# Kernel optimization log

Hardware: AMD Instinct MI355X
Metric: run time of the kernel (lower is better)

## Reference

```python
import jax, jax.numpy as jnp
import numpy as np

EMBED_DIM = 1024
NUM_HEADS = 16
HEAD_DIM = EMBED_DIM // NUM_HEADS


def layer_norm(x, gamma, beta, eps=1e-5):
    mu = jnp.mean(x, axis=-1, keepdims=True)
    var = jnp.var(x, axis=-1, keepdims=True)
    return (x - mu) * jax.lax.rsqrt(var + eps) * gamma + beta


def setup_inputs() -> dict:
    key = jax.random.key(0)
    ks = jax.random.split(key, 8)
    D = EMBED_DIM
    s = 1.0 / np.sqrt(D)
    x = jax.random.normal(ks[0], (2, 2048, D), dtype=jnp.float32)
    Wq = jax.random.uniform(ks[1], (D, D), jnp.float32, -s, s)
    Wk = jax.random.uniform(ks[2], (D, D), jnp.float32, -s, s)
    Wv = jax.random.uniform(ks[3], (D, D), jnp.float32, -s, s)
    W1 = jax.random.uniform(ks[4], (D, 4 * D), jnp.float32, -s, s)
    b1 = jnp.zeros((4 * D,), jnp.float32)
    W2 = jax.random.uniform(ks[5], (4 * D, D), jnp.float32, -1.0 / np.sqrt(4 * D), 1.0 / np.sqrt(4 * D))
    b2 = jnp.zeros((D,), jnp.float32)
    g1 = jnp.ones((D,), jnp.float32); be1 = jnp.zeros((D,), jnp.float32)
    g2 = jnp.ones((D,), jnp.float32); be2 = jnp.zeros((D,), jnp.float32)
    return {"x": x, "Wq": Wq, "Wk": Wk, "Wv": Wv, "W1": W1, "b1": b1,
            "W2": W2, "b2": b2, "g1": g1, "be1": be1, "g2": g2, "be2": be2}


def reference(x, Wq, Wk, Wv, W1, b1, W2, b2, g1, be1, g2, be2):
    B, S, D = x.shape
    H, Hd = NUM_HEADS, HEAD_DIM
    x_norm = layer_norm(x, g1, be1)
    # QKV projections (no bias), split into heads: [B, H, S, Hd]
    q = (x_norm @ Wq).reshape(B, S, H, Hd).transpose(0, 2, 1, 3)
    k = (x_norm @ Wk).reshape(B, S, H, Hd).transpose(0, 2, 1, 3)
    v = (x_norm @ Wv).reshape(B, S, H, Hd).transpose(0, 2, 1, 3)
    energy = jnp.einsum('bhqd,bhkd->bhqk', q, k)
    attn = jax.nn.softmax(energy / jnp.sqrt(jnp.float32(Hd)), axis=-1)
    out = jnp.einsum('bhqk,bhkd->bhqd', attn, v)
    attention = out.transpose(0, 2, 1, 3).reshape(B, S, D)
    x_res = attention + x
    x_norm2 = layer_norm(x_res, g2, be2)
    # Faithful quirk: FFN applied to x_res (not x_norm2)
    ffn_out = jax.nn.relu(x_res @ W1 + b1) @ W2 + b2
    return ffn_out + x_norm2
```

## Files before the change

kernel.cpp:

```cpp
#include <hip/hip_runtime.h>
#include <hip/hip_bf16.h>
#include <stdint.h>

typedef __hip_bfloat16 bf16;
typedef __attribute__((ext_vector_type(4))) float f32x4;
typedef __attribute__((ext_vector_type(8))) short s16x8;
typedef __attribute__((ext_vector_type(4))) short s16x4;

#define DEV static __device__ __forceinline__

DEV short f2bf(float f) {
  bf16 h = __float2bfloat16(f);
  short s;
  __builtin_memcpy(&s, &h, 2);
  return s;
}
DEV float bf2f(short s) {
  bf16 h;
  __builtin_memcpy(&h, &s, 2);
  return __bfloat162float(h);
}

__global__ __launch_bounds__(256) void transpose_cvt(
    const float* __restrict__ W, bf16* __restrict__ Wt, int K, int N)
{
  __shared__ float tile[32][33];
  const int n0 = blockIdx.x << 5;
  const int k0 = blockIdx.y << 5;
  const int tx = threadIdx.x & 31, ty = threadIdx.x >> 5;
#pragma unroll
  for (int i = 0; i < 4; ++i)
    tile[ty + i * 8][tx] = W[(size_t)(k0 + ty + i * 8) * N + n0 + tx];
  __syncthreads();
#pragma unroll
  for (int i = 0; i < 4; ++i)
    Wt[(size_t)(n0 + ty + i * 8) * K + k0 + tx] = __float2bfloat16(tile[tx][ty + i * 8]);
}

__global__ __launch_bounds__(256) void ln_bf16(
    const float* __restrict__ x, const float* __restrict__ g,
    const float* __restrict__ be, bf16* __restrict__ out)
{
  const int t = threadIdx.x;
  const size_t row = blockIdx.x;
  const float4 v = ((const float4*)(x + row * 1024))[t];
  float s = v.x + v.y + v.z + v.w;
  float ss = v.x * v.x + v.y * v.y + v.z * v.z + v.w * v.w;
#pragma unroll
  for (int off = 32; off > 0; off >>= 1) {
    s += __shfl_down(s, off);
    ss += __shfl_down(ss, off);
  }
  __shared__ float sh[8];
  const int wave = t >> 6, lane = t & 63;
  if (!lane) { sh[wave] = s; sh[4 + wave] = ss; }
  __syncthreads();
  s = sh[0] + sh[1] + sh[2] + sh[3];
  ss = sh[4] + sh[5] + sh[6] + sh[7];
  const float mean = s * (1.f / 1024.f);
  const float rstd = rsqrtf(ss * (1.f / 1024.f) - mean * mean + 1e-5f);
  const float4 gv = ((const float4*)g)[t];
  const float4 bv = ((const float4*)be)[t];
  s16x4 o;
  o[0] = f2bf((v.x - mean) * rstd * gv.x + bv.x);
  o[1] = f2bf((v.y - mean) * rstd * gv.y + bv.y);
  o[2] = f2bf((v.z - mean) * rstd * gv.z + bv.z);
  o[3] = f2bf((v.w - mean) * rstd * gv.w + bv.w);
  ((s16x4*)(out + row * 1024))[t] = o;
}

__global__ __launch_bounds__(256) void add_ln_bf16(
    const float* __restrict__ a, const float* __restrict__ x,
    const float* __restrict__ g, const float* __restrict__ be,
    bf16* __restrict__ xres, bf16* __restrict__ xnorm)
{
  const int t = threadIdx.x;
  const size_t row = blockIdx.x;
  const float4 av = ((const float4*)(a + row * 1024))[t];
  const float4 xv = ((const float4*)(x + row * 1024))[t];
  float4 v;
  v.x = av.x + xv.x; v.y = av.y + xv.y; v.z = av.z + xv.z; v.w = av.w + xv.w;
  float s = v.x + v.y + v.z + v.w;
  float ss = v.x * v.x + v.y * v.y + v.z * v.z + v.w * v.w;
#pragma unroll
  for (int off = 32; off > 0; off >>= 1) {
    s += __shfl_down(s, off);
    ss += __shfl_down(ss, off);
  }
  __shared__ float sh[8];
  const int wave = t >> 6, lane = t & 63;
  if (!lane) { sh[wave] = s; sh[4 + wave] = ss; }
  __syncthreads();
  s = sh[0] + sh[1] + sh[2] + sh[3];
  ss = sh[4] + sh[5] + sh[6] + sh[7];
  const float mean = s * (1.f / 1024.f);
  const float rstd = rsqrtf(ss * (1.f / 1024.f) - mean * mean + 1e-5f);
  const float4 gv = ((const float4*)g)[t];
  const float4 bv = ((const float4*)be)[t];
  s16x4 r, o;
  r[0] = f2bf(v.x); r[1] = f2bf(v.y); r[2] = f2bf(v.z); r[3] = f2bf(v.w);
  o[0] = f2bf((v.x - mean) * rstd * gv.x + bv.x);
  o[1] = f2bf((v.y - mean) * rstd * gv.y + bv.y);
  o[2] = f2bf((v.z - mean) * rstd * gv.z + bv.z);
  o[3] = f2bf((v.w - mean) * rstd * gv.w + bv.w);
  ((s16x4*)(xres + row * 1024))[t] = r;
  ((s16x4*)(xnorm + row * 1024))[t] = o;
}

template <int EPI>
__global__ __launch_bounds__(256) void gemm_bt(
    const bf16* __restrict__ A, const bf16* __restrict__ Bt,
    void* __restrict__ C, const float* __restrict__ bias,
    const bf16* __restrict__ add_bf16, int M, int N, int K)
{
  __shared__ bf16 sA0[128 * 64];
  __shared__ bf16 sB0[128 * 64];
  __shared__ bf16 sA1[128 * 64];
  __shared__ bf16 sB1[128 * 64];
  const int tid = threadIdx.x;
  const int wave = tid >> 6, lane = tid & 63;
  const int fr = lane & 15, fg = lane >> 4;
  const int f7 = fr & 7;
  const int wr = wave >> 1, wc = wave & 1;
  const int nbx = N >> 7;
  int bid = blockIdx.x;
  if ((gridDim.x & 7) == 0) {
    const int cpx = gridDim.x >> 3;
    bid = (bid & 7) * cpx + (bid >> 3);
  }
  const int brow = (bid / nbx) << 7;
  const int bcol = (bid % nbx) << 7;

  f32x4 acc[4][4] = {};

  const int rsub = lane >> 3;
  const int cl = (lane & 7) ^ rsub;
  size_t ga[4], gb[4];
  int la[4];
#pragma unroll
  for (int j = 0; j < 4; ++j) {
    const int r = wave * 32 + j * 8;
    ga[j] = (size_t)(brow + r + rsub) * K + cl * 8;
    gb[j] = (size_t)(bcol + r + rsub) * K + cl * 8;
    la[j] = r * 64;
  }

#define GSTAGE(SA, SB, kt)                                                     \
  do {                                                                         \
    _Pragma("unroll")                                                          \
    for (int jj = 0; jj < 4; ++jj) {                                           \
      __builtin_amdgcn_global_load_lds(                                        \
          (const __attribute__((address_space(1))) uint32_t*)(A + ga[jj] + (kt)), \
          (__attribute__((address_space(3))) uint32_t*)(&SA[la[jj]]), 16, 0, 0);  \
      __builtin_amdgcn_global_load_lds(                                        \
          (const __attribute__((address_space(1))) uint32_t*)(Bt + gb[jj] + (kt)),\
          (__attribute__((address_space(3))) uint32_t*)(&SB[la[jj]]), 16, 0, 0);  \
    }                                                                          \
  } while (0)

#define COMPUTE(SA, SB)                                                        \
  do {                                                                         \
    s16x8 af[4][2], bfr[4][2];                                                 \
    _Pragma("unroll")                                                          \
    for (int m = 0; m < 4; ++m)                                                \
      _Pragma("unroll")                                                        \
      for (int kk = 0; kk < 2; ++kk)                                           \
        af[m][kk] = *(const s16x8*)(&SA[(wr * 64 + m * 16 + fr) * 64 +         \
                                        (((kk * 4 + fg) ^ f7) << 3)]);         \
    _Pragma("unroll")                                                          \
    for (int n = 0; n < 4; ++n)                                                \
      _Pragma("unroll")                                                        \
      for (int kk = 0; kk < 2; ++kk)                                           \
        bfr[n][kk] = *(const s16x8*)(&SB[(wc * 64 + n * 16 + fr) * 64 +        \
                                         (((kk * 4 + fg) ^ f7) << 3)]);        \
    _Pragma("unroll")                                                          \
    for (int kk = 0; kk < 2; ++kk)                                             \
      _Pragma("unroll")                                                        \
      for (int m = 0; m < 4; ++m)                                              \
        _Pragma("unroll")                                                      \
        for (int n = 0; n < 4; ++n)                                            \
          acc[m][n] = __builtin_amdgcn_mfma_f32_16x16x32_bf16(                 \
              af[m][kk], bfr[n][kk], acc[m][n], 0, 0, 0);                      \
  } while (0)

  GSTAGE(sA0, sB0, 0);
  __syncthreads();

  int kt = 0;
  for (;;) {
    if (kt + 64 < K) {
      GSTAGE(sA1, sB1, kt + 64);
      COMPUTE(sA0, sB0);
      __syncthreads();
    } else {
      COMPUTE(sA0, sB0);
      break;
    }
    kt += 64;
    if (kt + 64 < K) {
      GSTAGE(sA0, sB0, kt + 64);
      COMPUTE(sA1, sB1);
      __syncthreads();
    } else {
      COMPUTE(sA1, sB1);
      break;
    }
    kt += 64;
  }
#undef GSTAGE
#undef COMPUTE

  const int crow = brow + wr * 64;
  const int ccol = bcol + wc * 64;
#pragma unroll
  for (int m = 0; m < 4; ++m) {
#pragma unroll
    for (int n = 0; n < 4; ++n) {
      const int col = ccol + n * 16 + fr;
#pragma unroll
      for (int j = 0; j < 4; ++j) {
        const int row = crow + m * 16 + fg * 4 + j;
        float v = acc[m][n][j];
        if (EPI == 0) {
          ((bf16*)C)[(size_t)row * N + col] = __float2bfloat16(v);
        } else if (EPI == 1) {
          v += bias[col];
          v = fmaxf(v, 0.f);
          ((bf16*)C)[(size_t)row * N + col] = __float2bfloat16(v);
        } else {
          float a;
          {
            bf16 hb = add_bf16[(size_t)row * N + col];
            a = __bfloat162float(hb);
          }
          ((float*)C)[(size_t)row * N + col] = v + bias[col] + a;
        }
      }
    }
  }
}

template <int EPI>
__global__ __launch_bounds__(512) void gemm512_bt(
    const bf16* __restrict__ A, const bf16* __restrict__ Bt,
    void* __restrict__ C, const float* __restrict__ bias, int M, int N, int K)
{
  __shared__ bf16 sA[3][256 * 64];
  __shared__ bf16 sB[3][128 * 64];
  const int tid = threadIdx.x;
  const int wave = tid >> 6, lane = tid & 63;
  const int fr = lane & 15, fg = lane >> 4;
  const int f7 = fr & 7;
  const int wr = wave >> 1, wc = wave & 1;
  const int nbx = N >> 7;
  int bid = blockIdx.x;
  if ((gridDim.x & 7) == 0) {
    const int cpx = gridDim.x >> 3;
    bid = (bid & 7) * cpx + (bid >> 3);
  }
  const int brow = (bid / nbx) << 8;
  const int bcol = (bid % nbx) << 7;

  f32x4 acc[4][4] = {};

  const int rsub = lane >> 3;
  const int cl = (lane & 7) ^ rsub;
  size_t ga[4], gb[2];
  int laA[4], laB[2];
#pragma unroll
  for (int j = 0; j < 4; ++j) {
    const int r = j * 64 + wave * 8;
    ga[j] = (size_t)(brow + r + rsub) * K + cl * 8;
    laA[j] = r * 64;
  }
#pragma unroll
  for (int j = 0; j < 2; ++j) {
    const int r = j * 64 + wave * 8;
    gb[j] = (size_t)(bcol + r + rsub) * K + cl * 8;
    laB[j] = r * 64;
  }

#define STG(bi, koff)                                                          \
  do {                                                                         \
    _Pragma("unroll")                                                          \
    for (int jj = 0; jj < 4; ++jj)                                             \
      __builtin_amdgcn_global_load_lds(                                        \
          (const __attribute__((address_space(1))) uint32_t*)(A + ga[jj] + (koff)), \
          (__attribute__((address_space(3))) uint32_t*)(&sA[bi][laA[jj]]), 16, 0, 0); \
    _Pragma("unroll")                                                          \
    for (int jj = 0; jj < 2; ++jj)                                             \
      __builtin_amdgcn_global_load_lds(                                        \
          (const __attribute__((address_space(1))) uint32_t*)(Bt + gb[jj] + (koff)),\
          (__attribute__((address_space(3))) uint32_t*)(&sB[bi][laB[jj]]), 16, 0, 0); \
  } while (0)

  const int nk = K >> 6;
  STG(0, 0);
  STG(1, 64);

  int cb = 0;
  for (int j = 0; j < nk; ++j) {
    if (j < nk - 1) {
      asm volatile("s_waitcnt vmcnt(6)" ::: "memory");
    } else {
      asm volatile("s_waitcnt vmcnt(0)" ::: "memory");
    }
    __builtin_amdgcn_s_barrier();
    if (j + 2 < nk) {
      const int tb = (cb + 2) % 3;
      STG(tb, (j + 2) * 64);
    }
    const bf16* SA = sA[cb];
    const bf16* SB = sB[cb];
    s16x8 af[4][2], bfr[4][2];
#pragma unroll
    for (int m = 0; m < 4; ++m)
#pragma unroll
      for (int kk = 0; kk < 2; ++kk)
        af[m][kk] = *(const s16x8*)(&SA[(wr * 64 + m * 16 + fr) * 64 +
                                        (((kk * 4 + fg) ^ f7) << 3)]);
#pragma unroll
    for (int n = 0; n < 4; ++n)
#pragma unroll
      for (int kk = 0; kk < 2; ++kk)
        bfr[n][kk] = *(const s16x8*)(&SB[(wc * 64 + n * 16 + fr) * 64 +
                                         (((kk * 4 + fg) ^ f7) << 3)]);
    __builtin_amdgcn_s_setprio(1);
#pragma unroll
    for (int kk = 0; kk < 2; ++kk)
#pragma unroll
      for (int m = 0; m < 4; ++m)
#pragma unroll
        for (int n = 0; n < 4; ++n)
          acc[m][n] = __builtin_amdgcn_mfma_f32_16x16x32_bf16(
              af[m][kk], bfr[n][kk], acc[m][n], 0, 0, 0);
    __builtin_amdgcn_s_setprio(0);
    cb = (cb + 1) % 3;
  }
#undef STG

  const int crow = brow + wr * 64;
  const int ccol = bcol + wc * 64;
#pragma unroll
  for (int m = 0; m < 4; ++m) {
#pragma unroll
    for (int n = 0; n < 4; ++n) {
      const int col = ccol + n * 16 + fr;
#pragma unroll
      for (int j = 0; j < 4; ++j) {
        const int row = crow + m * 16 + fg * 4 + j;
        float v = acc[m][n][j];
        if (EPI == 0) {
          ((bf16*)C)[(size_t)row * N + col] = __float2bfloat16(v);
        } else {
          v += bias[col];
          v = fmaxf(v, 0.f);
          ((bf16*)C)[(size_t)row * N + col] = __float2bfloat16(v);
        }
      }
    }
  }
}

__global__ __launch_bounds__(512, 4) void attn_fwd(
    const bf16* __restrict__ QK, const bf16* __restrict__ Vt,
    float* __restrict__ Out)
{
  const int LDK = 2048;
  const int qt = blockIdx.x;
  const int bh = blockIdx.y;
  const int b = bh >> 4, h = bh & 15;
  const int tid = threadIdx.x;
  const int wave = tid >> 6, lane = tid & 63;
  const int fr = lane & 15, fg = lane >> 4;
  const int f7 = fr & 7;

  const short* base = (const short*)QK + (size_t)b * 2048 * LDK;
  const short* Qp = base + h * 64;
  const short* Kp = base + 1024 + h * 64;
  const short* Vp = (const short*)Vt + (size_t)h * 64 * 4096 + b * 2048;
  const int q0 = qt * 128 + wave * 16;

  __shared__ short Kbuf[2][64 * 64];
  __shared__ short Vbuf[2][64 * 64];
  __shared__ short P_lds[8][16 * 72];
  short* Pw = P_lds[wave];

  const int rsub = lane >> 3;
  const int clog = (lane & 7) ^ rsub;
  const short* Ksrc = Kp + (size_t)(8 * wave + rsub) * LDK + clog * 8;
  const short* Vsrc = Vp + (size_t)(8 * wave + rsub) * 4096 + clog * 8;

  s16x8 qf0 = *(const s16x8*)(Qp + (size_t)(q0 + fr) * LDK + fg * 8);
  s16x8 qf1 = *(const s16x8*)(Qp + (size_t)(q0 + fr) * LDK + 32 + fg * 8);
#pragma unroll
  for (int i = 0; i < 8; ++i) {
    qf0[i] = f2bf(bf2f(qf0[i]) * 0.125f);
    qf1[i] = f2bf(bf2f(qf1[i]) * 0.125f);
  }

  f32x4 acc[4] = {};
  f32x4 mrow = {-1e30f, -1e30f, -1e30f, -1e30f};
  f32x4 lrow = {};

#define STAGE(bi, koff)                                                        \
  do {                                                                         \
    __builtin_amdgcn_global_load_lds(                                          \
        (const __attribute__((address_space(1))) uint32_t*)(Ksrc + (size_t)(koff) * LDK), \
        (__attribute__((address_space(3))) uint32_t*)(&Kbuf[bi][wave * 512]),  \
        16, 0, 0);                                                             \
    __builtin_amdgcn_global_load_lds(                                          \
        (const __attribute__((address_space(1))) uint32_t*)(Vsrc + (koff)),    \
        (__attribute__((address_space(3))) uint32_t*)(&Vbuf[bi][wave * 512]),  \
        16, 0, 0);                                                             \
  } while (0)

  int cur = 0;
  STAGE(0, 0);

  for (int kt = 0; kt < 2048; kt += 64) {
    if (kt + 64 < 2048) {
      STAGE(cur ^ 1, kt + 64);
      asm volatile("s_waitcnt vmcnt(2)" ::: "memory");
    } else {
      asm volatile("s_waitcnt vmcnt(0)" ::: "memory");
    }
    __builtin_amdgcn_s_barrier();
    __builtin_amdgcn_sched_barrier(0);

    const short* Kb = Kbuf[cur];
    const short* Vb = Vbuf[cur];

    f32x4 e[4];
    __builtin_amdgcn_s_setprio(1);
#pragma unroll
    for (int t = 0; t < 4; ++t) {
      const int ro = (t * 16 + fr) * 64;
      const s16x8 k0 = *(const s16x8*)(Kb + ro + ((fg ^ f7) << 3));
      const s16x8 k1 = *(const s16x8*)(Kb + ro + (((4 + fg) ^ f7) << 3));
      f32x4 z = {};
      z = __builtin_amdgcn_mfma_f32_16x16x32_bf16(qf0, k0, z, 0, 0, 0);
      z = __builtin_amdgcn_mfma_f32_16x16x32_bf16(qf1, k1, z, 0, 0, 0);
      e[t] = z;
    }
    __builtin_amdgcn_s_setprio(0);

    f32x4 lmx;
#pragma unroll
    for (int j = 0; j < 4; ++j)
      lmx[j] = fmaxf(fmaxf(e[0][j], e[1][j]), fmaxf(e[2][j], e[3][j]));
    const bool need = (lmx[0] > mrow[0] + 8.f) | (lmx[1] > mrow[1] + 8.f) |
                      (lmx[2] > mrow[2] + 8.f) | (lmx[3] > mrow[3] + 8.f);
    if (__any(need)) {
      f32x4 mx = lmx;
#pragma unroll
      for (int d = 1; d < 16; d <<= 1)
#pragma unroll
        for (int j = 0; j < 4; ++j) mx[j] = fmaxf(mx[j], __shfl_xor(mx[j], d));
#pragma unroll
      for (int j = 0; j < 4; ++j) {
        const float mn = fmaxf(mrow[j], mx[j]);
        const float al = __expf(mrow[j] - mn);
        lrow[j] *= al;
        mrow[j] = mn;
#pragma unroll
        for (int nn = 0; nn < 4; ++nn) acc[nn][j] *= al;
      }
    }

#pragma unroll
    for (int j = 0; j < 4; ++j) {
#pragma unroll
      for (int t = 0; t < 4; ++t) e[t][j] = __expf(e[t][j] - mrow[j]);
      lrow[j] += (e[0][j] + e[1][j]) + (e[2][j] + e[3][j]);
    }

#pragma unroll
    for (int t = 0; t < 4; ++t)
#pragma unroll
      for (int j = 0; j < 4; ++j)
        Pw[(fg * 4 + j) * 72 + t * 16 + fr] = f2bf(e[t][j]);
    const s16x8 pf0 = *(const s16x8*)(Pw + fr * 72 + fg * 8);
    const s16x8 pf1 = *(const s16x8*)(Pw + fr * 72 + 32 + fg * 8);

    __builtin_amdgcn_s_setprio(1);
#pragma unroll
    for (int nn = 0; nn < 4; ++nn) {
      const int ro = (nn * 16 + fr) * 64;
      const s16x8 vf0 = *(const s16x8*)(Vb + ro + ((fg ^ f7) << 3));
      const s16x8 vf1 = *(const s16x8*)(Vb + ro + (((4 + fg) ^ f7) << 3));
      acc[nn] = __builtin_amdgcn_mfma_f32_16x16x32_bf16(pf0, vf0, acc[nn], 0, 0, 0);
      acc[nn] = __builtin_amdgcn_mfma_f32_16x16x32_bf16(pf1, vf1, acc[nn], 0, 0, 0);
    }
    __builtin_amdgcn_s_setprio(0);

    __builtin_amdgcn_s_barrier();
    __builtin_amdgcn_sched_barrier(0);
    cur ^= 1;
  }
#undef STAGE

#pragma unroll
  for (int d = 1; d < 16; d <<= 1)
#pragma unroll
    for (int j = 0; j < 4; ++j) lrow[j] += __shfl_xor(lrow[j], d);
  f32x4 inv;
#pragma unroll
  for (int j = 0; j < 4; ++j) inv[j] = 1.0f / lrow[j];
  float* outp = Out + (size_t)(b * 2048 + q0) * 1024 + h * 64;
#pragma unroll
  for (int nn = 0; nn < 4; ++nn)
#pragma unroll
    for (int j = 0; j < 4; ++j)
      outp[(size_t)(fg * 4 + j) * 1024 + nn * 16 + fr] = acc[nn][j] * inv[j];
}

extern "C" void kernel_launch(void* const* d_in, const int* in_sizes, int n_in,
                              void* d_out, int out_size, void* d_ws, size_t ws_size,
                              hipStream_t stream)
{
  const float* x   = (const float*)d_in[0];
  const float* Wq  = (const float*)d_in[1];
  const float* Wk  = (const float*)d_in[2];
  const float* Wv  = (const float*)d_in[3];
  const float* W1  = (const float*)d_in[4];
  const float* b1  = (const float*)d_in[5];
  const float* W2  = (const float*)d_in[6];
  const float* b2  = (const float*)d_in[7];
  const float* g1  = (const float*)d_in[8];
  const float* be1 = (const float*)d_in[9];
  const float* g2  = (const float*)d_in[10];
  const float* be2 = (const float*)d_in[11];
  float* out = (float*)d_out;

  const int M = 4096, D = 1024, DF = 4096;

  bf16* Wqk_t = (bf16*)d_ws;
  bf16* Wv_t  = Wqk_t + (size_t)2048 * 1024;
  bf16* W1t   = Wv_t + (size_t)1024 * 1024;
  bf16* W2t   = W1t + (size_t)4096 * 1024;
  bf16* big   = W2t + (size_t)4096 * 1024;
  bf16* QK    = big;
  bf16* Vt    = big + (size_t)8 * 1024 * 1024;
  bf16* hbuf  = big;
  char* p2    = (char*)(big + (size_t)16 * 1024 * 1024);
  bf16* xnorm = (bf16*)p2;
  float* attnO = (float*)p2;
  char* p3    = p2 + (size_t)M * D * sizeof(float);
  bf16* xres  = (bf16*)p3;
  bf16* xnorm2 = xres + (size_t)M * D;

  transpose_cvt<<<dim3(32, 32), 256, 0, stream>>>(Wq, Wqk_t, D, D);
  transpose_cvt<<<dim3(32, 32), 256, 0, stream>>>(Wk, Wqk_t + (size_t)D * D, D, D);
  transpose_cvt<<<dim3(32, 32), 256, 0, stream>>>(Wv, Wv_t, D, D);
  transpose_cvt<<<dim3(128, 32), 256, 0, stream>>>(W1, W1t, D, DF);
  transpose_cvt<<<dim3(32, 128), 256, 0, stream>>>(W2, W2t, DF, D);
  ln_bf16<<<M, 256, 0, stream>>>(x, g1, be1, xnorm);
  gemm512_bt<0><<<(M / 256) * (2048 / 128), 512, 0, stream>>>(
      xnorm, Wqk_t, QK, nullptr, M, 2048, D);
  gemm_bt<0><<<(D / 128) * (M / 128), 256, 0, stream>>>(
      Wv_t, xnorm, Vt, nullptr, nullptr, D, M, D);
  attn_fwd<<<dim3(16, 32), 512, 0, stream>>>(QK, Vt, attnO);
  add_ln_bf16<<<M, 256, 0, stream>>>(attnO, x, g2, be2, xres, xnorm2);
  gemm512_bt<1><<<(M / 256) * (DF / 128), 512, 0, stream>>>(
      xres, W1t, hbuf, b1, M, DF, D);
  gemm_bt<2><<<(M / 128) * (D / 128), 256, 0, stream>>>(
      hbuf, W2t, out, b2, xnorm2, M, D, DF);
}
```

Measured before the change: 254.7 us.

## Use 256x256 tiled double-buffered GEMM for FFN1 and 128-tile GEMM for QK

```diff
diff --git a/kernel.cpp b/kernel.cpp
--- a/kernel.cpp
+++ b/kernel.cpp
@@ -145,15 +145,15 @@
     la[j] = r * 64;
   }
 
-#define GSTAGE(SA, SB, kt)                                                     \
+#define GSTAGE(SA, SB, koff)                                                   \
   do {                                                                         \
     _Pragma("unroll")                                                          \
     for (int jj = 0; jj < 4; ++jj) {                                           \
       __builtin_amdgcn_global_load_lds(                                        \
-          (const __attribute__((address_space(1))) uint32_t*)(A + ga[jj] + (kt)), \
+          (const __attribute__((address_space(1))) uint32_t*)(A + ga[jj] + (koff)), \
           (__attribute__((address_space(3))) uint32_t*)(&SA[la[jj]]), 16, 0, 0);  \
       __builtin_amdgcn_global_load_lds(                                        \
-          (const __attribute__((address_space(1))) uint32_t*)(Bt + gb[jj] + (kt)),\
+          (const __attribute__((address_space(1))) uint32_t*)(Bt + gb[jj] + (koff)),\
           (__attribute__((address_space(3))) uint32_t*)(&SB[la[jj]]), 16, 0, 0);  \
     }                                                                          \
   } while (0)
@@ -241,108 +241,120 @@
 }
 
 template <int EPI>
-__global__ __launch_bounds__(512) void gemm512_bt(
+__global__ __launch_bounds__(512) void gemm256_bt(
     const bf16* __restrict__ A, const bf16* __restrict__ Bt,
     void* __restrict__ C, const float* __restrict__ bias, int M, int N, int K)
 {
-  __shared__ bf16 sA[3][256 * 64];
-  __shared__ bf16 sB[3][128 * 64];
+  __shared__ bf16 sA0[256 * 64];
+  __shared__ bf16 sB0[256 * 64];
+  __shared__ bf16 sA1[256 * 64];
+  __shared__ bf16 sB1[256 * 64];
   const int tid = threadIdx.x;
   const int wave = tid >> 6, lane = tid & 63;
   const int fr = lane & 15, fg = lane >> 4;
   const int f7 = fr & 7;
-  const int wr = wave >> 1, wc = wave & 1;
-  const int nbx = N >> 7;
+  const int wr = wave >> 2, wc = wave & 3;
+  const int nbx = N >> 8;
   int bid = blockIdx.x;
   if ((gridDim.x & 7) == 0) {
     const int cpx = gridDim.x >> 3;
     bid = (bid & 7) * cpx + (bid >> 3);
   }
   const int brow = (bid / nbx) << 8;
-  const int bcol = (bid % nbx) << 7;
-
-  f32x4 acc[4][4] = {};
+  const int bcol = (bid % nbx) << 8;
+
+  f32x4 acc[8][4] = {};
 
   const int rsub = lane >> 3;
   const int cl = (lane & 7) ^ rsub;
-  size_t ga[4], gb[2];
-  int laA[4], laB[2];
+  size_t ga[4], gb[4];
+  int la[4];
 #pragma unroll
   for (int j = 0; j < 4; ++j) {
     const int r = j * 64 + wave * 8;
     ga[j] = (size_t)(brow + r + rsub) * K + cl * 8;
-    laA[j] = r * 64;
-  }
-#pragma unroll
-  for (int j = 0; j < 2; ++j) {
-    const int r = j * 64 + wave * 8;
     gb[j] = (size_t)(bcol + r + rsub) * K + cl * 8;
-    laB[j] = r * 64;
-  }
-
-#define STG(bi, koff)                                                          \
+    la[j] = r * 64;
+  }
+
+#define STG6(SA, SB, koff)                                                     \
   do {                                                                         \
     _Pragma("unroll")                                                          \
-    for (int jj = 0; jj < 4; ++jj)                                             \
+    for (int jj = 0; jj < 4; ++jj) {                                           \
       __builtin_amdgcn_global_load_lds(                                        \
           (const __attribute__((address_space(1))) uint32_t*)(A + ga[jj] + (koff)), \
-          (__attribute__((address_space(3))) uint32_t*)(&sA[bi][laA[jj]]), 16, 0, 0); \
-    _Pragma("unroll")                                                          \
-    for (int jj = 0; jj < 2; ++jj)                                             \
+          (__attribute__((address_space(3))) uint32_t*)(&SA[la[jj]]), 16, 0, 0);  \
       __builtin_amdgcn_global_load_lds(                                        \
           (const __attribute__((address_space(1))) uint32_t*)(Bt + gb[jj] + (koff)),\
-          (__attribute__((address_space(3))) uint32_t*)(&sB[bi][laB[jj]]), 16, 0, 0); \
+          (__attribute__((address_space(3))) uint32_t*)(&SB[la[jj]]), 16, 0, 0);  \
+    }                                                                          \
   } while (0)
 
-  const int nk = K >> 6;
-  STG(0, 0);
-  STG(1, 64);
-
-  int cb = 0;
-  for (int j = 0; j < nk; ++j) {
-    if (j < nk - 1) {
-      asm volatile("s_waitcnt vmcnt(6)" ::: "memory");
+#define CMP6(SA, SB)                                                           \
+  do {                                                                         \
+    s16x8 bfr[4][2];                                                           \
+    _Pragma("unroll")                                                          \
+    for (int n = 0; n < 4; ++n)                                                \
+      _Pragma("unroll")                                                        \
+      for (int kk = 0; kk < 2; ++kk)                                           \
+        bfr[n][kk] = *(const s16x8*)(&SB[(wc * 64 + n * 16 + fr) * 64 +        \
+                                         (((kk * 4 + fg) ^ f7) << 3)]);        \
+    __builtin_amdgcn_s_setprio(1);                                             \
+    _Pragma("unroll")                                                          \
+    for (int m = 0; m < 8; ++m) {                                              \
+      s16x8 afm[2];                                                            \
+      _Pragma("unroll")                                                        \
+      for (int kk = 0; kk < 2; ++kk)                                           \
+        afm[kk] = *(const s16x8*)(&SA[(wr * 128 + m * 16 + fr) * 64 +          \
+                                      (((kk * 4 + fg) ^ f7) << 3)]);           \
+      _Pragma("unroll")                                                        \
+      for (int kk = 0; kk < 2; ++kk)                                           \
+        _Pragma("unroll")                                                      \
+        for (int n = 0; n < 4; ++n)                                            \
+          acc[m][n] = __builtin_amdgcn_mfma_f32_16x16x32_bf16(                 \
+              afm[kk], bfr[n][kk], acc[m][n], 0, 0, 0);                        \
+    }                                                                          \
+    __builtin_amdgcn_s_setprio(0);                                             \
+  } while (0)
+
+  STG6(sA0, sB0, 0);
+
+  int kt = 0;
+  for (;;) {
+    if (kt + 64 < K) {
+      STG6(sA1, sB1, kt + 64);
+      asm volatile("s_waitcnt vmcnt(8)" ::: "memory");
     } else {
       asm volatile("s_waitcnt vmcnt(0)" ::: "memory");
     }
     __builtin_amdgcn_s_barrier();
-    if (j + 2 < nk) {
-      const int tb = (cb + 2) % 3;
-      STG(tb, (j + 2) * 64);
-    }
-    const bf16* SA = sA[cb];
-    const bf16* SB = sB[cb];
-    s16x8 af[4][2], bfr[4][2];
-#pragma unroll
-    for (int m = 0; m < 4; ++m)
-#pragma unroll
-      for (int kk = 0; kk < 2; ++kk)
-        af[m][kk] = *(const s16x8*)(&SA[(wr * 64 + m * 16 + fr) * 64 +
-                                        (((kk * 4 + fg) ^ f7) << 3)]);
-#pragma unroll
-    for (int n = 0; n < 4; ++n)
-#pragma unroll
-      for (int kk = 0; kk < 2; ++kk)
-        bfr[n][kk] = *(const s16x8*)(&SB[(wc * 64 + n * 16 + fr) * 64 +
-                                         (((kk * 4 + fg) ^ f7) << 3)]);
-    __builtin_amdgcn_s_setprio(1);
-#pragma unroll
-    for (int kk = 0; kk < 2; ++kk)
-#pragma unroll
-      for (int m = 0; m < 4; ++m)
-#pragma unroll
-        for (int n = 0; n < 4; ++n)
-          acc[m][n] = __builtin_amdgcn_mfma_f32_16x16x32_bf16(
-              af[m][kk], bfr[n][kk], acc[m][n], 0, 0, 0);
-    __builtin_amdgcn_s_setprio(0);
-    cb = (cb + 1) % 3;
-  }
-#undef STG
-
-  const int crow = brow + wr * 64;
+    __builtin_amdgcn_sched_barrier(0);
+    CMP6(sA0, sB0);
+    if (kt + 64 >= K) break;
+    __builtin_amdgcn_s_barrier();
+    __builtin_amdgcn_sched_barrier(0);
+    kt += 64;
+    if (kt + 64 < K) {
+      STG6(sA0, sB0, kt + 64);
+      asm volatile("s_waitcnt vmcnt(8)" ::: "memory");
+    } else {
+      asm volatile("s_waitcnt vmcnt(0)" ::: "memory");
+    }
+    __builtin_amdgcn_s_barrier();
+    __builtin_amdgcn_sched_barrier(0);
+    CMP6(sA1, sB1);
+    if (kt + 64 >= K) break;
+    __builtin_amdgcn_s_barrier();
+    __builtin_amdgcn_sched_barrier(0);
+    kt += 64;
+  }
+#undef STG6
+#undef CMP6
+
+  const int crow = brow + wr * 128;
   const int ccol = bcol + wc * 64;
 #pragma unroll
-  for (int m = 0; m < 4; ++m) {
+  for (int m = 0; m < 8; ++m) {
 #pragma unroll
     for (int n = 0; n < 4; ++n) {
       const int col = ccol + n * 16 + fr;
@@ -556,13 +568,13 @@
   transpose_cvt<<<dim3(128, 32), 256, 0, stream>>>(W1, W1t, D, DF);
   transpose_cvt<<<dim3(32, 128), 256, 0, stream>>>(W2, W2t, DF, D);
   ln_bf16<<<M, 256, 0, stream>>>(x, g1, be1, xnorm);
-  gemm512_bt<0><<<(M / 256) * (2048 / 128), 512, 0, stream>>>(
-      xnorm, Wqk_t, QK, nullptr, M, 2048, D);
+  gemm_bt<0><<<(M / 128) * (2048 / 128), 256, 0, stream>>>(
+      xnorm, Wqk_t, QK, nullptr, nullptr, M, 2048, D);
   gemm_bt<0><<<(D / 128) * (M / 128), 256, 0, stream>>>(
       Wv_t, xnorm, Vt, nullptr, nullptr, D, M, D);
   attn_fwd<<<dim3(16, 32), 512, 0, stream>>>(QK, Vt, attnO);
   add_ln_bf16<<<M, 256, 0, stream>>>(attnO, x, g2, be2, xres, xnorm2);
-  gemm512_bt<1><<<(M / 256) * (DF / 128), 512, 0, stream>>>(
+  gemm256_bt<1><<<(M / 256) * (DF / 256), 512, 0, stream>>>(
       xres, W1t, hbuf, b1, M, DF, D);
   gemm_bt<2><<<(M / 128) * (D / 128), 256, 0, stream>>>(
       hbuf, W2t, out, b2, xnorm2, M, D, DF);
```

New measurement: 237.9 us. 6.6% less time.
